# Kernel tuning notes

Hardware: AMD Instinct MI355X
Metric: run time of the kernel (lower is better)

The kernel has to match this reference:

```python
import jax, jax.numpy as jnp
import numpy as np

EPS = 0.1
MAX_ITER = 10
N, IN_SIZE, IN_DIM = 16, 1024, 1024
HEADS, OUT_SIZE, OUT_DIM = 4, 128, 1024


def xavier(key, shape):
    fan_in, fan_out = shape[-1], int(np.prod(shape[:-1]))
    lim = float(np.sqrt(6.0 / (fan_in + fan_out)))
    return jax.random.uniform(key, shape, jnp.float32, -lim, lim)


def setup_inputs() -> dict:
    key = jax.random.key(0)
    k1, k2, k3 = jax.random.split(key, 3)
    x = jax.random.normal(k1, (N, IN_SIZE, IN_DIM), jnp.float32)
    ot_weight = xavier(k2, (HEADS, OUT_SIZE, IN_DIM))
    lin_w = xavier(k3, (OUT_DIM, HEADS * IN_DIM))
    lin_b = jnp.zeros((OUT_DIM,), jnp.float32)
    return {"x": x, "ot_weight": ot_weight, "lin_w": lin_w, "lin_b": lin_b}


def log_sinkhorn(K, max_iter):
    # K: [B, in_size, out_size] (already divided by eps)
    B, in_size, out_size = K.shape
    a = jnp.log(jnp.asarray(out_size / in_size, K.dtype))
    u = jnp.zeros((B, in_size), K.dtype)
    v = jnp.zeros((B, out_size), K.dtype)

    def body(carry, _):
        u, v = carry
        u = a - jax.nn.logsumexp(K + u[:, :, None] + v[:, None, :], axis=-1)
        v = -jax.nn.logsumexp(K + u[:, :, None] + v[:, None, :], axis=-2)
        return (u, v), None

    (u, v), _ = jax.lax.scan(body, (u, v), None, length=max_iter)
    return jnp.exp(K + u[:, :, None] + v[:, None, :])  # transport plan T


def reference(x, ot_weight, lin_w, lin_b):
    n, in_size, in_dim = x.shape
    m, out_size, _ = ot_weight.shape
    # similarity / eps : [n, m, in_size, out_size]
    K = jnp.einsum('nid,msd->nmis', x, ot_weight) / EPS
    T = log_sinkhorn(K.reshape(n * m, in_size, out_size), MAX_ITER)
    T = T.reshape(n, m, in_size, out_size)
    # weighted aggregation: [n, out_size, m, in_dim] -> [n, out_size, m*in_dim]
    feat = jnp.einsum('nmis,nid->nsmd', T, x).reshape(n, out_size, m * in_dim)
    # Linear + ReLU (Dropout is identity in eval mode)
    out = jax.nn.relu(feat @ lin_w.T + lin_b)
    return out
```

## Files before the change

kernel.cpp:

```cpp
#include <hip/hip_runtime.h>
#include <math.h>

#define EPSV 0.1f
#define MAX_ITER 10
constexpr int NB       = 16;
constexpr int IN_SIZE  = 1024;
constexpr int IN_DIM   = 1024;
constexpr int HEADS    = 4;
constexpr int OUT_SIZE = 128;
constexpr int OUT_DIM  = 1024;

typedef __attribute__((ext_vector_type(8))) _Float16 f16x8;
typedef __attribute__((ext_vector_type(4))) float f32x4;

__device__ __forceinline__ unsigned cvth2(float lo, float hi) {
    _Float16 a = (_Float16)lo, b = (_Float16)hi;
    unsigned short ua = *(unsigned short*)&a, ub = *(unsigned short*)&b;
    return (unsigned)ua | ((unsigned)ub << 16);
}
__device__ __forceinline__ unsigned short cvth1(float f) {
    _Float16 a = (_Float16)f;
    return *(unsigned short*)&a;
}
__device__ __forceinline__ unsigned short bf16rne(float f) {
    unsigned a = __float_as_uint(f);
    return (unsigned short)((a + 0x7fffu + ((a >> 16) & 1u)) >> 16);
}
__device__ __forceinline__ void glds16(const void* g, void* l) {
    __builtin_amdgcn_global_load_lds(
        (const __attribute__((address_space(1))) unsigned int*)g,
        (__attribute__((address_space(3))) unsigned int*)l, 16, 0, 0);
}

template<bool B_F32, int CMODE, int NF, bool AKBLK, bool SWAP>
__global__ __launch_bounds__(256)
void mfma_gemm(const void* __restrict__ Ap, const void* __restrict__ Bp,
               const float* __restrict__ bias, void* __restrict__ Cp,
               int K, int lda, int ldb, int ldc, int div,
               long AsN, long AsM, long BsN, long BsM, long CsN, long CsM,
               long AkStride, float alpha)
{
    constexpr int BN   = NF * 32;
    constexpr int BSTR = B_F32 ? 40 : 32;
    const int z  = SWAP ? blockIdx.x : blockIdx.z;
    const int n0 = (SWAP ? blockIdx.z : blockIdx.x) * BN;
    const long aoff = (long)(z / div) * AsN + (long)(z % div) * AsM;
    const long boff = (long)(z / div) * BsN + (long)(z % div) * BsM;
    const long coff = (long)(z / div) * CsN + (long)(z % div) * CsM;

    __shared__ short As[128 * 32];
    __shared__ short Bs[BN * BSTR];

    const int t = threadIdx.x;
    const int lane = t & 63;
    const int w = t >> 6, wr = w >> 1, wc = w & 1;

    f32x4 acc[4][NF];
    #pragma unroll
    for (int i = 0; i < 4; ++i)
        #pragma unroll
        for (int j = 0; j < NF; ++j) { acc[i][j].x = 0.f; acc[i][j].y = 0.f; acc[i][j].z = 0.f; acc[i][j].w = 0.f; }

    const int lrow = lane >> 2, lce = (lane & 3) * 8;

    for (int k0 = 0; k0 < K; k0 += 32) {
        const long abase = AKBLK ? aoff + (long)(k0 >> 10) * AkStride + (k0 & 1023)
                                 : aoff + k0;
        const long bbase = boff + k0;
        #pragma unroll
        for (int j = 0; j < 2; ++j) {
            const int row0 = (w * 2 + j) * 16;
            glds16((const short*)Ap + abase + (long)(row0 + lrow) * lda + lce,
                   &As[row0 * 32]);
        }
        if (B_F32) {
            #pragma unroll
            for (int itr = 0; itr < BN / 64; ++itr) {
                const int idx = itr * 256 + t;
                const int row = idx >> 2, kq = idx & 3;
                const float* s = (const float*)Bp + bbase + (long)(n0 + row) * ldb + kq * 8;
                const float4 f0 = *(const float4*)s, f1 = *(const float4*)(s + 4);
                uint4 p;
                p.x = cvth2(f0.x, f0.y); p.y = cvth2(f0.z, f0.w);
                p.z = cvth2(f1.x, f1.y); p.w = cvth2(f1.z, f1.w);
                *(uint4*)&Bs[row * BSTR + kq * 8] = p;
            }
        } else {
            #pragma unroll
            for (int j = 0; j < BN / 64; ++j) {
                const int row0 = (w * (BN / 64) + j) * 16;
                glds16((const short*)Bp + bbase + (long)(n0 + row0 + lrow) * ldb + lce,
                       &Bs[row0 * 32]);
            }
        }
        __syncthreads();

        f16x8 af[4], bfr[NF];
        #pragma unroll
        for (int mi = 0; mi < 4; ++mi)
            af[mi] = *(const f16x8*)&As[(wr * 64 + mi * 16 + (lane & 15)) * 32 + (lane >> 4) * 8];
        #pragma unroll
        for (int ni = 0; ni < NF; ++ni)
            bfr[ni] = *(const f16x8*)&Bs[(wc * (BN / 2) + ni * 16 + (lane & 15)) * BSTR + (lane >> 4) * 8];
        #pragma unroll
        for (int mi = 0; mi < 4; ++mi)
            #pragma unroll
            for (int ni = 0; ni < NF; ++ni)
                acc[mi][ni] = __builtin_amdgcn_mfma_f32_16x16x32_f16(af[mi], bfr[ni], acc[mi][ni], 0, 0, 0);
        __syncthreads();
    }

    #pragma unroll
    for (int mi = 0; mi < 4; ++mi) {
        #pragma unroll
        for (int ni = 0; ni < NF; ++ni) {
            #pragma unroll
            for (int j = 0; j < 4; ++j) {
                const int row = wr * 64 + mi * 16 + (lane >> 4) * 4 + j;
                const int col = n0 + wc * (BN / 2) + ni * 16 + (lane & 15);
                float v = acc[mi][ni][j] * alpha;
                if (CMODE == 2) { v += bias[col]; v = fmaxf(v, 0.f); }
                if (CMODE == 2 || CMODE == 4) ((float*)Cp)[coff + (long)row * ldc + col] = v;
                else ((unsigned short*)Cp)[coff + (long)row * ldc + col] = cvth1(v);
            }
        }
    }
}

__global__ __launch_bounds__(256)
void splitk_reduce(const float* __restrict__ part, const float* __restrict__ bias,
                   float* __restrict__ out)
{
    const long idx = ((long)blockIdx.x * 256 + threadIdx.x) * 4;
    const int o = (int)(idx & 1023);
    const float4 p0 = *(const float4*)(part + idx);
    const float4 p1 = *(const float4*)(part + 2097152 + idx);
    const float4 p2 = *(const float4*)(part + 2 * 2097152 + idx);
    const float4 p3 = *(const float4*)(part + 3 * 2097152 + idx);
    const float4 bv = *(const float4*)(bias + o);
    float4 r;
    r.x = fmaxf(p0.x + p1.x + p2.x + p3.x + bv.x, 0.f);
    r.y = fmaxf(p0.y + p1.y + p2.y + p3.y + bv.y, 0.f);
    r.z = fmaxf(p0.z + p1.z + p2.z + p3.z + bv.z, 0.f);
    r.w = fmaxf(p0.w + p1.w + p2.w + p3.w + bv.w, 0.f);
    *(float4*)(out + idx) = r;
}

__global__ __launch_bounds__(256)
void cvt_f16(const float* __restrict__ in, unsigned short* __restrict__ out)
{
    const long i8 = ((long)blockIdx.x * 256 + threadIdx.x) * 8;
    const float4 f0 = *(const float4*)(in + i8), f1 = *(const float4*)(in + i8 + 4);
    uint4 p;
    p.x = cvth2(f0.x, f0.y); p.y = cvth2(f0.z, f0.w);
    p.z = cvth2(f1.x, f1.y); p.w = cvth2(f1.z, f1.w);
    *(uint4*)(out + i8) = p;
}

__global__ __launch_bounds__(256)
void gemm1_exp(const unsigned short* __restrict__ otwH,
               const unsigned short* __restrict__ xH,
               unsigned short* __restrict__ ekb, float* __restrict__ MiB)
{
    const int zb = blockIdx.x;
    const int nn = zb >> 2, mm = zb & 3;
    const unsigned short* A = otwH + (long)mm * (OUT_SIZE * IN_DIM);
    const unsigned short* B = xH + (long)nn * (IN_SIZE * IN_DIM);
    const int n0 = blockIdx.z * 128;

    __shared__ short As[128 * 32];
    __shared__ short Bs[128 * 32];
    __shared__ float colmax[2][128];

    const int t = threadIdx.x;
    const int lane = t & 63;
    const int w = t >> 6, wr = w >> 1, wc = w & 1;
    const int lrow = lane >> 2, lce = (lane & 3) * 8;

    f32x4 acc[4][4];
    #pragma unroll
    for (int i = 0; i < 4; ++i)
        #pragma unroll
        for (int j = 0; j < 4; ++j) { acc[i][j].x = 0.f; acc[i][j].y = 0.f; acc[i][j].z = 0.f; acc[i][j].w = 0.f; }

    for (int k0 = 0; k0 < 1024; k0 += 32) {
        #pragma unroll
        for (int j = 0; j < 2; ++j) {
            const int row0 = (w * 2 + j) * 16;
            glds16(A + (long)(row0 + lrow) * 1024 + k0 + lce, &As[row0 * 32]);
        }
        #pragma unroll
        for (int j = 0; j < 2; ++j) {
            const int row0 = (w * 2 + j) * 16;
            glds16(B + (long)(n0 + row0 + lrow) * 1024 + k0 + lce, &Bs[row0 * 32]);
        }
        __syncthreads();

        f16x8 af[4], bfr[4];
        #pragma unroll
        for (int mi = 0; mi < 4; ++mi)
            af[mi] = *(const f16x8*)&As[(wr * 64 + mi * 16 + (lane & 15)) * 32 + (lane >> 4) * 8];
        #pragma unroll
        for (int ni = 0; ni < 4; ++ni)
            bfr[ni] = *(const f16x8*)&Bs[(wc * 64 + ni * 16 + (lane & 15)) * 32 + (lane >> 4) * 8];
        #pragma unroll
        for (int mi = 0; mi < 4; ++mi)
            #pragma unroll
            for (int ni = 0; ni < 4; ++ni)
                acc[mi][ni] = __builtin_amdgcn_mfma_f32_16x16x32_f16(af[mi], bfr[ni], acc[mi][ni], 0, 0, 0);
        __syncthreads();
    }

    float lm[4];
    #pragma unroll
    for (int ni = 0; ni < 4; ++ni) {
        float mx = -INFINITY;
        #pragma unroll
        for (int mi = 0; mi < 4; ++mi)
            #pragma unroll
            for (int j = 0; j < 4; ++j) mx = fmaxf(mx, acc[mi][ni][j]);
        mx *= 10.0f;
        mx = fmaxf(mx, __shfl_xor(mx, 16, 64));
        mx = fmaxf(mx, __shfl_xor(mx, 32, 64));
        lm[ni] = mx;
    }
    if ((lane >> 4) == 0) {
        #pragma unroll
        for (int ni = 0; ni < 4; ++ni) colmax[wr][wc * 64 + ni * 16 + lane] = lm[ni];
    }
    __syncthreads();
    float cm[4];
    #pragma unroll
    for (int ni = 0; ni < 4; ++ni) {
        const int c = wc * 64 + ni * 16 + (lane & 15);
        cm[ni] = fmaxf(colmax[0][c], colmax[1][c]);
    }
    if (wr == 0 && (lane >> 4) == 0) {
        #pragma unroll
        for (int ni = 0; ni < 4; ++ni)
            MiB[(long)zb * 1024 + n0 + wc * 64 + ni * 16 + lane] = cm[ni];
    }
    unsigned short* ekz = ekb + (long)zb * (OUT_SIZE * IN_SIZE);
    #pragma unroll
    for (int mi = 0; mi < 4; ++mi) {
        #pragma unroll
        for (int ni = 0; ni < 4; ++ni) {
            const int col = n0 + wc * 64 + ni * 16 + (lane & 15);
            #pragma unroll
            for (int j = 0; j < 4; ++j) {
                const int row = wr * 64 + mi * 16 + (lane >> 4) * 4 + j;
                ekz[(long)row * 1024 + col] = bf16rne(__expf(fmaf(acc[mi][ni][j], 10.f, -cm[ni])));
            }
        }
    }
}

__global__ __launch_bounds__(256)
void transpose_cvt(const float* __restrict__ x, unsigned short* __restrict__ xT)
{
    const int n = blockIdx.z, i0 = blockIdx.y * 64, d0 = blockIdx.x * 64;
    const float* xs = x + (long)n * (IN_SIZE * IN_DIM);
    unsigned short* xo = xT + (long)n * (IN_SIZE * IN_DIM);
    __shared__ float tile[64][65];
    const int t = threadIdx.x;
    const int r = t >> 4, c4 = (t & 15) * 4;
    #pragma unroll
    for (int rr = 0; rr < 4; ++rr) {
        const float4 v = *(const float4*)(xs + (long)(i0 + rr * 16 + r) * IN_DIM + d0 + c4);
        *(float4*)&tile[rr * 16 + r][c4] = v;
    }
    __syncthreads();
    #pragma unroll
    for (int rr = 0; rr < 4; ++rr) {
        const int dl = rr * 16 + r;
        ushort4 o;
        o.x = cvth1(tile[c4 + 0][dl]); o.y = cvth1(tile[c4 + 1][dl]);
        o.z = cvth1(tile[c4 + 2][dl]); o.w = cvth1(tile[c4 + 3][dl]);
        *(ushort4*)(xo + (long)(d0 + dl) * IN_SIZE + i0 + c4) = o;
    }
}

__global__ __launch_bounds__(1024)
void sinkhorn_split(unsigned short* __restrict__ ekb,
                    const float* __restrict__ MiB,
                    float* __restrict__ xchg, unsigned int* __restrict__ ctr)
{
    const int b = blockIdx.x;
    const int q = blockIdx.z;
    const int t = threadIdx.x;
    const int lane = t & 63, w = t >> 6;

    __shared__ unsigned ekw[128 * 129];
    __shared__ float part_u[8][256];
    __shared__ float part_v[8][128];
    __shared__ float eu_l[256];
    __shared__ float v_s[128], ev_s[128];
    __shared__ float red8[8];
    __shared__ float wg_s;

    {
        const unsigned short* src = ekb + (long)b * 131072 + q * 256;
        #pragma unroll
        for (int j = 0; j < 4; ++j) {
            const int idx = t + 1024 * j;
            const int s = idx >> 5, c8 = (idx & 31) * 8;
            const uint4 p = *(const uint4*)(src + (long)s * 1024 + c8);
            const int bd = s * 129 + (c8 >> 1);
            ekw[bd] = p.x; ekw[bd + 1] = p.y; ekw[bd + 2] = p.z; ekw[bd + 3] = p.w;
        }
    }
    float mi_t = 0.f, u_reg = 0.f, w_t = 0.f;
    if (t < 256) mi_t = MiB[(long)b * 1024 + q * 256 + t];
    if (t < 128) { v_s[t] = 0.f; ev_s[t] = 1.0f; }
    __syncthreads();

    const float A0 = -2.0794415416798357f;
    float vmx = 0.f;

    for (int it = 0; it < MAX_ITER; ++it) {
        {
            const int p = t & 127, sq = t >> 7;
            float s0 = 0.f, s1 = 0.f;
            #pragma unroll
            for (int j = 0; j < 16; ++j) {
                const int s = sq * 16 + j;
                const unsigned e = ekw[s * 129 + p];
                const float evv = ev_s[s];
                s0 = fmaf(__uint_as_float(e << 16),          evv, s0);
                s1 = fmaf(__uint_as_float(e & 0xffff0000u),  evv, s1);
            }
            part_u[sq][2 * p]     = s0;
            part_u[sq][2 * p + 1] = s1;
        }
        __syncthreads();

        if (t < 256) {
            float S = part_u[0][t];
            #pragma unroll
            for (int g = 1; g < 8; ++g) S += part_u[g][t];
            const float un = A0 - u_reg - mi_t - vmx - __logf(S);
            u_reg = un;
            w_t = mi_t + un;
            float wl = w_t;
            #pragma unroll
            for (int m = 1; m < 64; m <<= 1) wl = fmaxf(wl, __shfl_xor(wl, m, 64));
            if (lane == 0) red8[4 + w] = wl;
        }
        __syncthreads();
        const float wmx_l = fmaxf(fmaxf(red8[4], red8[5]), fmaxf(red8[6], red8[7]));
        if (t < 256) eu_l[t] = __expf(w_t - wmx_l);
        __syncthreads();

        {
            const int s = t & 127, g = t >> 7;
            float acc = 0.f;
            #pragma unroll
            for (int j = 0; j < 16; ++j) {
                const int p = 16 * g + j;
                const unsigned e = ekw[s * 129 + p];
                const float2 eup = *(const float2*)&eu_l[2 * p];
                acc = fmaf(__uint_as_float(e << 16),         eup.x, acc);
                acc = fmaf(__uint_as_float(e & 0xffff0000u), eup.y, acc);
            }
            part_v[g][s] = acc;
        }
        __syncthreads();

        float* slot = xchg + ((long)(b * MAX_ITER + it) * 4 + q) * 160;
        if (t < 128) {
            float cp_l = part_v[0][t];
            #pragma unroll
            for (int g = 1; g < 8; ++g) cp_l += part_v[g][t];
            __hip_atomic_store(slot + t, cp_l, __ATOMIC_RELAXED, __HIP_MEMORY_SCOPE_AGENT);
        }
        if (t == 0)
            __hip_atomic_store(slot + 128, wmx_l, __ATOMIC_RELAXED, __HIP_MEMORY_SCOPE_AGENT);
        __syncthreads();
        if (t == 0) {
            unsigned int* c = ctr + b * MAX_ITER + it;
            __hip_atomic_fetch_add(c, 1u, __ATOMIC_RELEASE, __HIP_MEMORY_SCOPE_AGENT);
            while (__hip_atomic_load(c, __ATOMIC_RELAXED, __HIP_MEMORY_SCOPE_AGENT) < 4u) {}
            (void)__hip_atomic_load(c, __ATOMIC_ACQUIRE, __HIP_MEMORY_SCOPE_AGENT);
        }
        __syncthreads();

        if (t < 128) {
            float* base = xchg + (long)(b * MAX_ITER + it) * 4 * 160;
            const float w0 = __hip_atomic_load(base + 0 * 160 + 128, __ATOMIC_RELAXED, __HIP_MEMORY_SCOPE_AGENT);
            const float w1 = __hip_atomic_load(base + 1 * 160 + 128, __ATOMIC_RELAXED, __HIP_MEMORY_SCOPE_AGENT);
            const float w2 = __hip_atomic_load(base + 2 * 160 + 128, __ATOMIC_RELAXED, __HIP_MEMORY_SCOPE_AGENT);
            const float w3 = __hip_atomic_load(base + 3 * 160 + 128, __ATOMIC_RELAXED, __HIP_MEMORY_SCOPE_AGENT);
            const float wg = fmaxf(fmaxf(w0, w1), fmaxf(w2, w3));
            const float c0 = __hip_atomic_load(base + 0 * 160 + t, __ATOMIC_RELAXED, __HIP_MEMORY_SCOPE_AGENT);
            const float c1 = __hip_atomic_load(base + 1 * 160 + t, __ATOMIC_RELAXED, __HIP_MEMORY_SCOPE_AGENT);
            const float c2 = __hip_atomic_load(base + 2 * 160 + t, __ATOMIC_RELAXED, __HIP_MEMORY_SCOPE_AGENT);
            const float c3 = __hip_atomic_load(base + 3 * 160 + t, __ATOMIC_RELAXED, __HIP_MEMORY_SCOPE_AGENT);
            const float cp = c0 * __expf(w0 - wg) + c1 * __expf(w1 - wg)
                           + c2 * __expf(w2 - wg) + c3 * __expf(w3 - wg);
            const float vn = -v_s[t] - wg - __logf(cp);
            v_s[t] = vn;
            if (t == 0) wg_s = wg;
            float xv = vn;
            #pragma unroll
            for (int m = 1; m < 64; m <<= 1) xv = fmaxf(xv, __shfl_xor(xv, m, 64));
            if (lane == 0) red8[w] = xv;
        }
        __syncthreads();
        vmx = fmaxf(red8[0], red8[1]);
        if (t < 128) ev_s[t] = __expf(v_s[t] - vmx);
        __syncthreads();
    }

    const float wg = wg_s;
    if (t < 256) eu_l[t] = __expf(w_t - wg);
    if (t < 128) ev_s[t] = __expf(v_s[t] + wg);
    __syncthreads();
    unsigned short* To = ekb + (long)b * 131072 + q * 256;
    #pragma unroll
    for (int j = 0; j < 16; ++j) {
        const int idx = t + 1024 * j;
        const int s  = idx >> 7;
        const int ip = idx & 127;
        const unsigned e = ekw[s * 129 + ip];
        const float2 eup = *(const float2*)&eu_l[2 * ip];
        const float ec = ev_s[s];
        const float lo = __uint_as_float(e << 16)         * eup.x * ec;
        const float hi = __uint_as_float(e & 0xffff0000u) * eup.y * ec;
        *(unsigned*)(To + (long)s * 1024 + ip * 2) = cvth2(lo, hi);
    }
}

extern "C" void kernel_launch(void* const* d_in, const int* in_sizes, int n_in,
                              void* d_out, int out_size, void* d_ws, size_t ws_size,
                              hipStream_t stream)
{
    const float* x     = (const float*)d_in[0];
    const float* otw   = (const float*)d_in[1];
    const float* lin_w = (const float*)d_in[2];
    const float* lin_b = (const float*)d_in[3];
    float* out = (float*)d_out;

    unsigned short* xH   = (unsigned short*)d_ws;
    unsigned short* xT   = (unsigned short*)d_ws;
    unsigned short* ekb  = xH + 16777216;
    unsigned short* feat = ekb + 8388608;
    float* partial = (float*)d_ws;
    float* MiB  = (float*)d_out;
    float* xchg = MiB + 131072;
    unsigned int* ctrB = (unsigned int*)(MiB + 655360);
    unsigned short* otwH = (unsigned short*)(MiB + 786432);

    hipMemsetAsync(ctrB, 0, 64 * MAX_ITER * sizeof(unsigned int), stream);

    cvt_f16<<<dim3(256), 256, 0, stream>>>(otw, otwH);
    cvt_f16<<<dim3(8192), 256, 0, stream>>>(x, xH);

    gemm1_exp<<<dim3(64, 1, 8), 256, 0, stream>>>(otwH, xH, ekb, MiB);

    transpose_cvt<<<dim3(16, 16, NB), 256, 0, stream>>>(x, xT);

    sinkhorn_split<<<dim3(64, 1, 4), 1024, 0, stream>>>(ekb, MiB, xchg, ctrB);

    mfma_gemm<false, 1, 4, false, true><<<dim3(64, 1, 8), 256, 0, stream>>>(
        ekb, xT, nullptr, feat,
        1024, 1024, 1024, 1024, 4,
        524288, 131072, 1048576, 0, 524288, 131072, 0, 1.0f);

    mfma_gemm<true, 4, 2, false, false><<<dim3(16, 1, 64), 256, 0, stream>>>(
        feat, lin_w, nullptr, partial,
        1024, 1024, 4096, 1024, 16,
        131072, 524288, 1024, 0, 2097152, 131072, 0, 1.0f);

    splitk_reduce<<<dim3(2048), 256, 0, stream>>>(partial, lin_b, out);
}
```

Baseline: 208.2 us.

## Double-buffer LDS tiles in GEMMs and shrink sinkhorn v-update to one wave

The generic MFMA GEMM and the first similarity GEMM now use two LDS buffers, so the next K-slice is loaded while MFMAs run on the current one. This removes one barrier per iteration and hides load latency, at the cost of twice the shared memory, which may reduce occupancy. Separately, the cross-block v-update in the sinkhorn loop is done by a single wave handling two entries per lane. That lets the max reduction and exp happen in-wave and drops one __syncthreads per iteration.

```diff
diff --git a/kernel.cpp b/kernel.cpp
--- a/kernel.cpp
+++ b/kernel.cpp
@@ -48,22 +48,15 @@
     const long boff = (long)(z / div) * BsN + (long)(z % div) * BsM;
     const long coff = (long)(z / div) * CsN + (long)(z % div) * CsM;
 
-    __shared__ short As[128 * 32];
-    __shared__ short Bs[BN * BSTR];
+    __shared__ short As[2][128 * 32];
+    __shared__ short Bs[2][BN * BSTR];
 
     const int t = threadIdx.x;
     const int lane = t & 63;
     const int w = t >> 6, wr = w >> 1, wc = w & 1;
-
-    f32x4 acc[4][NF];
-    #pragma unroll
-    for (int i = 0; i < 4; ++i)
-        #pragma unroll
-        for (int j = 0; j < NF; ++j) { acc[i][j].x = 0.f; acc[i][j].y = 0.f; acc[i][j].z = 0.f; acc[i][j].w = 0.f; }
-
     const int lrow = lane >> 2, lce = (lane & 3) * 8;
 
-    for (int k0 = 0; k0 < K; k0 += 32) {
+    auto stage = [&](int buf, int k0) {
         const long abase = AKBLK ? aoff + (long)(k0 >> 10) * AkStride + (k0 & 1023)
                                  : aoff + k0;
         const long bbase = boff + k0;
@@ -71,7 +64,7 @@
         for (int j = 0; j < 2; ++j) {
             const int row0 = (w * 2 + j) * 16;
             glds16((const short*)Ap + abase + (long)(row0 + lrow) * lda + lce,
-                   &As[row0 * 32]);
+                   &As[buf][row0 * 32]);
         }
         if (B_F32) {
             #pragma unroll
@@ -83,31 +76,45 @@
                 uint4 p;
                 p.x = cvth2(f0.x, f0.y); p.y = cvth2(f0.z, f0.w);
                 p.z = cvth2(f1.x, f1.y); p.w = cvth2(f1.z, f1.w);
-                *(uint4*)&Bs[row * BSTR + kq * 8] = p;
+                *(uint4*)&Bs[buf][row * BSTR + kq * 8] = p;
             }
         } else {
             #pragma unroll
             for (int j = 0; j < BN / 64; ++j) {
                 const int row0 = (w * (BN / 64) + j) * 16;
                 glds16((const short*)Bp + bbase + (long)(n0 + row0 + lrow) * ldb + lce,
-                       &Bs[row0 * 32]);
-            }
-        }
-        __syncthreads();
+                       &Bs[buf][row0 * 32]);
+            }
+        }
+    };
+
+    f32x4 acc[4][NF];
+    #pragma unroll
+    for (int i = 0; i < 4; ++i)
+        #pragma unroll
+        for (int j = 0; j < NF; ++j) { acc[i][j].x = 0.f; acc[i][j].y = 0.f; acc[i][j].z = 0.f; acc[i][j].w = 0.f; }
+
+    stage(0, 0);
+    __syncthreads();
+    int cur = 0;
+
+    for (int k0 = 0; k0 < K; k0 += 32) {
+        if (k0 + 32 < K) stage(cur ^ 1, k0 + 32);
 
         f16x8 af[4], bfr[NF];
         #pragma unroll
         for (int mi = 0; mi < 4; ++mi)
-            af[mi] = *(const f16x8*)&As[(wr * 64 + mi * 16 + (lane & 15)) * 32 + (lane >> 4) * 8];
+            af[mi] = *(const f16x8*)&As[cur][(wr * 64 + mi * 16 + (lane & 15)) * 32 + (lane >> 4) * 8];
         #pragma unroll
         for (int ni = 0; ni < NF; ++ni)
-            bfr[ni] = *(const f16x8*)&Bs[(wc * (BN / 2) + ni * 16 + (lane & 15)) * BSTR + (lane >> 4) * 8];
+            bfr[ni] = *(const f16x8*)&Bs[cur][(wc * (BN / 2) + ni * 16 + (lane & 15)) * BSTR + (lane >> 4) * 8];
         #pragma unroll
         for (int mi = 0; mi < 4; ++mi)
             #pragma unroll
             for (int ni = 0; ni < NF; ++ni)
                 acc[mi][ni] = __builtin_amdgcn_mfma_f32_16x16x32_f16(af[mi], bfr[ni], acc[mi][ni], 0, 0, 0);
         __syncthreads();
+        cur ^= 1;
     }
 
     #pragma unroll
@@ -168,8 +175,8 @@
     const unsigned short* B = xH + (long)nn * (IN_SIZE * IN_DIM);
     const int n0 = blockIdx.z * 128;
 
-    __shared__ short As[128 * 32];
-    __shared__ short Bs[128 * 32];
+    __shared__ short As[2][128 * 32];
+    __shared__ short Bs[2][128 * 32];
     __shared__ float colmax[2][128];
 
     const int t = threadIdx.x;
@@ -177,38 +184,46 @@
     const int w = t >> 6, wr = w >> 1, wc = w & 1;
     const int lrow = lane >> 2, lce = (lane & 3) * 8;
 
-    f32x4 acc[4][4];
-    #pragma unroll
-    for (int i = 0; i < 4; ++i)
-        #pragma unroll
-        for (int j = 0; j < 4; ++j) { acc[i][j].x = 0.f; acc[i][j].y = 0.f; acc[i][j].z = 0.f; acc[i][j].w = 0.f; }
-
-    for (int k0 = 0; k0 < 1024; k0 += 32) {
+    auto stage = [&](int buf, int k0) {
         #pragma unroll
         for (int j = 0; j < 2; ++j) {
             const int row0 = (w * 2 + j) * 16;
-            glds16(A + (long)(row0 + lrow) * 1024 + k0 + lce, &As[row0 * 32]);
+            glds16(A + (long)(row0 + lrow) * 1024 + k0 + lce, &As[buf][row0 * 32]);
         }
         #pragma unroll
         for (int j = 0; j < 2; ++j) {
             const int row0 = (w * 2 + j) * 16;
-            glds16(B + (long)(n0 + row0 + lrow) * 1024 + k0 + lce, &Bs[row0 * 32]);
-        }
-        __syncthreads();
+            glds16(B + (long)(n0 + row0 + lrow) * 1024 + k0 + lce, &Bs[buf][row0 * 32]);
+        }
+    };
+
+    f32x4 acc[4][4];
+    #pragma unroll
+    for (int i = 0; i < 4; ++i)
+        #pragma unroll
+        for (int j = 0; j < 4; ++j) { acc[i][j].x = 0.f; acc[i][j].y = 0.f; acc[i][j].z = 0.f; acc[i][j].w = 0.f; }
+
+    stage(0, 0);
+    __syncthreads();
+    int cur = 0;
+
+    for (int k0 = 0; k0 < 1024; k0 += 32) {
+        if (k0 + 32 < 1024) stage(cur ^ 1, k0 + 32);
 
         f16x8 af[4], bfr[4];
         #pragma unroll
         for (int mi = 0; mi < 4; ++mi)
-            af[mi] = *(const f16x8*)&As[(wr * 64 + mi * 16 + (lane & 15)) * 32 + (lane >> 4) * 8];
+            af[mi] = *(const f16x8*)&As[cur][(wr * 64 + mi * 16 + (lane & 15)) * 32 + (lane >> 4) * 8];
         #pragma unroll
         for (int ni = 0; ni < 4; ++ni)
-            bfr[ni] = *(const f16x8*)&Bs[(wc * 64 + ni * 16 + (lane & 15)) * 32 + (lane >> 4) * 8];
+            bfr[ni] = *(const f16x8*)&Bs[cur][(wc * 64 + ni * 16 + (lane & 15)) * 32 + (lane >> 4) * 8];
         #pragma unroll
         for (int mi = 0; mi < 4; ++mi)
             #pragma unroll
             for (int ni = 0; ni < 4; ++ni)
                 acc[mi][ni] = __builtin_amdgcn_mfma_f32_16x16x32_f16(af[mi], bfr[ni], acc[mi][ni], 0, 0, 0);
         __syncthreads();
+        cur ^= 1;
     }
 
     float lm[4];
@@ -384,31 +399,37 @@
         }
         __syncthreads();
 
-        if (t < 128) {
+        if (t < 64) {
             float* base = xchg + (long)(b * MAX_ITER + it) * 4 * 160;
             const float w0 = __hip_atomic_load(base + 0 * 160 + 128, __ATOMIC_RELAXED, __HIP_MEMORY_SCOPE_AGENT);
             const float w1 = __hip_atomic_load(base + 1 * 160 + 128, __ATOMIC_RELAXED, __HIP_MEMORY_SCOPE_AGENT);
             const float w2 = __hip_atomic_load(base + 2 * 160 + 128, __ATOMIC_RELAXED, __HIP_MEMORY_SCOPE_AGENT);
             const float w3 = __hip_atomic_load(base + 3 * 160 + 128, __ATOMIC_RELAXED, __HIP_MEMORY_SCOPE_AGENT);
             const float wg = fmaxf(fmaxf(w0, w1), fmaxf(w2, w3));
-            const float c0 = __hip_atomic_load(base + 0 * 160 + t, __ATOMIC_RELAXED, __HIP_MEMORY_SCOPE_AGENT);
-            const float c1 = __hip_atomic_load(base + 1 * 160 + t, __ATOMIC_RELAXED, __HIP_MEMORY_SCOPE_AGENT);
-            const float c2 = __hip_atomic_load(base + 2 * 160 + t, __ATOMIC_RELAXED, __HIP_MEMORY_SCOPE_AGENT);
-            const float c3 = __hip_atomic_load(base + 3 * 160 + t, __ATOMIC_RELAXED, __HIP_MEMORY_SCOPE_AGENT);
-            const float cp = c0 * __expf(w0 - wg) + c1 * __expf(w1 - wg)
-                           + c2 * __expf(w2 - wg) + c3 * __expf(w3 - wg);
-            const float vn = -v_s[t] - wg - __logf(cp);
-            v_s[t] = vn;
+            const float e0 = __expf(w0 - wg), e1 = __expf(w1 - wg);
+            const float e2 = __expf(w2 - wg), e3 = __expf(w3 - wg);
+            float vn[2];
+            #pragma unroll
+            for (int h = 0; h < 2; ++h) {
+                const int s = t + 64 * h;
+                const float c0 = __hip_atomic_load(base + 0 * 160 + s, __ATOMIC_RELAXED, __HIP_MEMORY_SCOPE_AGENT);
+                const float c1 = __hip_atomic_load(base + 1 * 160 + s, __ATOMIC_RELAXED, __HIP_MEMORY_SCOPE_AGENT);
+                const float c2 = __hip_atomic_load(base + 2 * 160 + s, __ATOMIC_RELAXED, __HIP_MEMORY_SCOPE_AGENT);
+                const float c3 = __hip_atomic_load(base + 3 * 160 + s, __ATOMIC_RELAXED, __HIP_MEMORY_SCOPE_AGENT);
+                const float cp = c0 * e0 + c1 * e1 + c2 * e2 + c3 * e3;
+                vn[h] = -v_s[s] - wg - __logf(cp);
+                v_s[s] = vn[h];
+            }
             if (t == 0) wg_s = wg;
-            float xv = vn;
+            float xv = fmaxf(vn[0], vn[1]);
             #pragma unroll
             for (int m = 1; m < 64; m <<= 1) xv = fmaxf(xv, __shfl_xor(xv, m, 64));
-            if (lane == 0) red8[w] = xv;
-        }
-        __syncthreads();
-        vmx = fmaxf(red8[0], red8[1]);
-        if (t < 128) ev_s[t] = __expf(v_s[t] - vmx);
-        __syncthreads();
+            ev_s[t]      = __expf(vn[0] - xv);
+            ev_s[t + 64] = __expf(vn[1] - xv);
+            if (t == 0) red8[0] = xv;
+        }
+        __syncthreads();
+        vmx = red8[0];
     }
 
     const float wg = wg_s;
```

Measured after the change: 211.0 us. No clear change (+1.3%).

## Double-buffer GEMM LDS tiles and fuse x f16 conversion into gemm1

Applied to the files above, without the earlier changes.

Both GEMM kernels now use two LDS buffers and issue the next K-tile's loads before computing on the current one, so global loads overlap with MFMA work. gemm1_exp now reads fp32 x directly and converts it to f16 while staging into padded LDS rows. This removes the separate cvt_f16 pass over x along with its 32MB f16 write and re-read. In exchange LDS use doubles per block, which may lower occupancy, and gemm1 now reads twice the bytes of x through synchronous register loads instead of async global-to-LDS copies.

```diff
diff --git a/kernel.cpp b/kernel.cpp
--- a/kernel.cpp
+++ b/kernel.cpp
@@ -48,22 +48,15 @@
     const long boff = (long)(z / div) * BsN + (long)(z % div) * BsM;
     const long coff = (long)(z / div) * CsN + (long)(z % div) * CsM;
 
-    __shared__ short As[128 * 32];
-    __shared__ short Bs[BN * BSTR];
+    __shared__ short As[2][128 * 32];
+    __shared__ short Bs[2][BN * BSTR];
 
     const int t = threadIdx.x;
     const int lane = t & 63;
     const int w = t >> 6, wr = w >> 1, wc = w & 1;
-
-    f32x4 acc[4][NF];
-    #pragma unroll
-    for (int i = 0; i < 4; ++i)
-        #pragma unroll
-        for (int j = 0; j < NF; ++j) { acc[i][j].x = 0.f; acc[i][j].y = 0.f; acc[i][j].z = 0.f; acc[i][j].w = 0.f; }
-
     const int lrow = lane >> 2, lce = (lane & 3) * 8;
 
-    for (int k0 = 0; k0 < K; k0 += 32) {
+    auto stage = [&](int buf, int k0) {
         const long abase = AKBLK ? aoff + (long)(k0 >> 10) * AkStride + (k0 & 1023)
                                  : aoff + k0;
         const long bbase = boff + k0;
@@ -71,7 +64,7 @@
         for (int j = 0; j < 2; ++j) {
             const int row0 = (w * 2 + j) * 16;
             glds16((const short*)Ap + abase + (long)(row0 + lrow) * lda + lce,
-                   &As[row0 * 32]);
+                   &As[buf][row0 * 32]);
         }
         if (B_F32) {
             #pragma unroll
@@ -83,31 +76,45 @@
                 uint4 p;
                 p.x = cvth2(f0.x, f0.y); p.y = cvth2(f0.z, f0.w);
                 p.z = cvth2(f1.x, f1.y); p.w = cvth2(f1.z, f1.w);
-                *(uint4*)&Bs[row * BSTR + kq * 8] = p;
+                *(uint4*)&Bs[buf][row * BSTR + kq * 8] = p;
             }
         } else {
             #pragma unroll
             for (int j = 0; j < BN / 64; ++j) {
                 const int row0 = (w * (BN / 64) + j) * 16;
                 glds16((const short*)Bp + bbase + (long)(n0 + row0 + lrow) * ldb + lce,
-                       &Bs[row0 * 32]);
-            }
-        }
-        __syncthreads();
+                       &Bs[buf][row0 * 32]);
+            }
+        }
+    };
+
+    f32x4 acc[4][NF];
+    #pragma unroll
+    for (int i = 0; i < 4; ++i)
+        #pragma unroll
+        for (int j = 0; j < NF; ++j) { acc[i][j].x = 0.f; acc[i][j].y = 0.f; acc[i][j].z = 0.f; acc[i][j].w = 0.f; }
+
+    stage(0, 0);
+    __syncthreads();
+    int cur = 0;
+
+    for (int k0 = 0; k0 < K; k0 += 32) {
+        if (k0 + 32 < K) stage(cur ^ 1, k0 + 32);
 
         f16x8 af[4], bfr[NF];
         #pragma unroll
         for (int mi = 0; mi < 4; ++mi)
-            af[mi] = *(const f16x8*)&As[(wr * 64 + mi * 16 + (lane & 15)) * 32 + (lane >> 4) * 8];
+            af[mi] = *(const f16x8*)&As[cur][(wr * 64 + mi * 16 + (lane & 15)) * 32 + (lane >> 4) * 8];
         #pragma unroll
         for (int ni = 0; ni < NF; ++ni)
-            bfr[ni] = *(const f16x8*)&Bs[(wc * (BN / 2) + ni * 16 + (lane & 15)) * BSTR + (lane >> 4) * 8];
+            bfr[ni] = *(const f16x8*)&Bs[cur][(wc * (BN / 2) + ni * 16 + (lane & 15)) * BSTR + (lane >> 4) * 8];
         #pragma unroll
         for (int mi = 0; mi < 4; ++mi)
             #pragma unroll
             for (int ni = 0; ni < NF; ++ni)
                 acc[mi][ni] = __builtin_amdgcn_mfma_f32_16x16x32_f16(af[mi], bfr[ni], acc[mi][ni], 0, 0, 0);
         __syncthreads();
+        cur ^= 1;
     }
 
     #pragma unroll
@@ -158,18 +165,17 @@
 }
 
 __global__ __launch_bounds__(256)
-void gemm1_exp(const unsigned short* __restrict__ otwH,
-               const unsigned short* __restrict__ xH,
+void gemm1_exp(const unsigned short* __restrict__ otwH, const float* __restrict__ x,
                unsigned short* __restrict__ ekb, float* __restrict__ MiB)
 {
     const int zb = blockIdx.x;
     const int nn = zb >> 2, mm = zb & 3;
     const unsigned short* A = otwH + (long)mm * (OUT_SIZE * IN_DIM);
-    const unsigned short* B = xH + (long)nn * (IN_SIZE * IN_DIM);
+    const float* B = x + (long)nn * (IN_SIZE * IN_DIM);
     const int n0 = blockIdx.z * 128;
 
-    __shared__ short As[128 * 32];
-    __shared__ short Bs[128 * 32];
+    __shared__ short As[2][128 * 32];
+    __shared__ short Bs[2][128 * 40];
     __shared__ float colmax[2][128];
 
     const int t = threadIdx.x;
@@ -177,38 +183,52 @@
     const int w = t >> 6, wr = w >> 1, wc = w & 1;
     const int lrow = lane >> 2, lce = (lane & 3) * 8;
 
-    f32x4 acc[4][4];
-    #pragma unroll
-    for (int i = 0; i < 4; ++i)
-        #pragma unroll
-        for (int j = 0; j < 4; ++j) { acc[i][j].x = 0.f; acc[i][j].y = 0.f; acc[i][j].z = 0.f; acc[i][j].w = 0.f; }
-
-    for (int k0 = 0; k0 < 1024; k0 += 32) {
+    auto stage = [&](int buf, int k0) {
         #pragma unroll
         for (int j = 0; j < 2; ++j) {
             const int row0 = (w * 2 + j) * 16;
-            glds16(A + (long)(row0 + lrow) * 1024 + k0 + lce, &As[row0 * 32]);
-        }
-        #pragma unroll
-        for (int j = 0; j < 2; ++j) {
-            const int row0 = (w * 2 + j) * 16;
-            glds16(B + (long)(n0 + row0 + lrow) * 1024 + k0 + lce, &Bs[row0 * 32]);
-        }
-        __syncthreads();
+            glds16(A + (long)(row0 + lrow) * 1024 + k0 + lce, &As[buf][row0 * 32]);
+        }
+        #pragma unroll
+        for (int itr = 0; itr < 2; ++itr) {
+            const int idx = itr * 256 + t;
+            const int row = idx >> 2, kq = idx & 3;
+            const float* s = B + (long)(n0 + row) * 1024 + k0 + kq * 8;
+            const float4 f0 = *(const float4*)s, f1 = *(const float4*)(s + 4);
+            uint4 p;
+            p.x = cvth2(f0.x, f0.y); p.y = cvth2(f0.z, f0.w);
+            p.z = cvth2(f1.x, f1.y); p.w = cvth2(f1.z, f1.w);
+            *(uint4*)&Bs[buf][row * 40 + kq * 8] = p;
+        }
+    };
+
+    f32x4 acc[4][4];
+    #pragma unroll
+    for (int i = 0; i < 4; ++i)
+        #pragma unroll
+        for (int j = 0; j < 4; ++j) { acc[i][j].x = 0.f; acc[i][j].y = 0.f; acc[i][j].z = 0.f; acc[i][j].w = 0.f; }
+
+    stage(0, 0);
+    __syncthreads();
+    int cur = 0;
+
+    for (int k0 = 0; k0 < 1024; k0 += 32) {
+        if (k0 + 32 < 1024) stage(cur ^ 1, k0 + 32);
 
         f16x8 af[4], bfr[4];
         #pragma unroll
         for (int mi = 0; mi < 4; ++mi)
-            af[mi] = *(const f16x8*)&As[(wr * 64 + mi * 16 + (lane & 15)) * 32 + (lane >> 4) * 8];
+            af[mi] = *(const f16x8*)&As[cur][(wr * 64 + mi * 16 + (lane & 15)) * 32 + (lane >> 4) * 8];
         #pragma unroll
         for (int ni = 0; ni < 4; ++ni)
-            bfr[ni] = *(const f16x8*)&Bs[(wc * 64 + ni * 16 + (lane & 15)) * 32 + (lane >> 4) * 8];
+            bfr[ni] = *(const f16x8*)&Bs[cur][(wc * 64 + ni * 16 + (lane & 15)) * 40 + (lane >> 4) * 8];
         #pragma unroll
         for (int mi = 0; mi < 4; ++mi)
             #pragma unroll
             for (int ni = 0; ni < 4; ++ni)
                 acc[mi][ni] = __builtin_amdgcn_mfma_f32_16x16x32_f16(af[mi], bfr[ni], acc[mi][ni], 0, 0, 0);
         __syncthreads();
+        cur ^= 1;
     }
 
     float lm[4];
@@ -440,9 +460,8 @@
     const float* lin_b = (const float*)d_in[3];
     float* out = (float*)d_out;
 
-    unsigned short* xH   = (unsigned short*)d_ws;
     unsigned short* xT   = (unsigned short*)d_ws;
-    unsigned short* ekb  = xH + 16777216;
+    unsigned short* ekb  = xT + 16777216;
     unsigned short* feat = ekb + 8388608;
     float* partial = (float*)d_ws;
     float* MiB  = (float*)d_out;
@@ -453,9 +472,8 @@
     hipMemsetAsync(ctrB, 0, 64 * MAX_ITER * sizeof(unsigned int), stream);
 
     cvt_f16<<<dim3(256), 256, 0, stream>>>(otw, otwH);
-    cvt_f16<<<dim3(8192), 256, 0, stream>>>(x, xH);
-
-    gemm1_exp<<<dim3(64, 1, 8), 256, 0, stream>>>(otwH, xH, ekb, MiB);
+
+    gemm1_exp<<<dim3(64, 1, 8), 256, 0, stream>>>(otwH, x, ekb, MiB);
 
     transpose_cvt<<<dim3(16, 16, NB), 256, 0, stream>>>(x, xT);
 
```

Result: no change. 205.0 us (-1.6%).
